# Optimization experiments

Hardware: AMD Instinct MI355X
Metric: run time of the kernel (lower is better)

Reference implementation:

```python
import jax, jax.numpy as jnp
import numpy as np
import math

B, S, H, K = 512, 200, 256, 16

def setup_inputs() -> dict:
    key = jax.random.key(0)
    ks = jax.random.split(key, 8)
    scale = 1.0 / math.sqrt(H)
    return {
        "input_tensor": jax.random.normal(ks[0], (B, S, H), dtype=jnp.float32),
        "item_mask": jax.random.randint(ks[1], (B, S, 1), 0, 2) > 0,
        "time_f_w_matrix": jax.random.uniform(ks[2], (B, S, 1), dtype=jnp.float32),
        "W1": jax.random.normal(ks[3], (H, H), dtype=jnp.float32) * scale,
        "b1": jnp.zeros((H,), dtype=jnp.float32),
        "W2": jax.random.normal(ks[4], (H, H), dtype=jnp.float32) * scale,
        "b2": jnp.zeros((H,), dtype=jnp.float32),
        "W3": jax.random.normal(ks[5], (H, K), dtype=jnp.float32) * scale,
    }

def reference(input_tensor, item_mask, time_f_w_matrix, W1, b1, W2, b2, W3):
    # small MLP: two Linear+ReLU then bias-free Linear to k_interests
    h = jax.nn.relu(jnp.einsum('bsh,hd->bsd', input_tensor, W1) + b1)
    h = jax.nn.relu(jnp.einsum('bsh,hd->bsd', h, W2) + b2)
    D = jnp.einsum('bsh,hk->bsk', h, W3)              # [B,S,K]
    D = jax.nn.softmax(D, axis=-1)                    # softmax over interests
    mask = item_mask[:, :, 0:1]                       # [B,S,1] bool, broadcast over K
    D = jnp.where(mask, D, jnp.float32(-10000.0))
    D = D / jnp.float32(math.sqrt(K))
    D = jax.nn.softmax(D, axis=-2)                    # softmax over sequence
    D = time_f_w_matrix[:, :, 0:1] * D                # time weighting
    # einsum 'nij,nik->nkj': pool items into K interest vectors
    return jnp.einsum('bsh,bsk->bkh', input_tensor, D)
```

## Files before the change

### kernel.cpp

```cpp
#include <hip/hip_runtime.h>
#include <math.h>

#define HDIM 256
#define KDIM 16
#define SDIM 200
#define BDIM 512
#define NROWS (BDIM * SDIM)
#define TM 64

typedef __bf16 bf16x8 __attribute__((ext_vector_type(8)));
typedef __bf16 bf16x4 __attribute__((ext_vector_type(4)));
typedef float  f32x4  __attribute__((ext_vector_type(4)));

__global__ __launch_bounds__(256) void pack_w_kernel(
    const float* __restrict__ src, __bf16* __restrict__ hi,
    __bf16* __restrict__ lo, int lgN)
{
    int idx = blockIdx.x * 256 + threadIdx.x;
    int N = 1 << lgN;
    int k = idx >> lgN;
    int n = idx & (N - 1);
    float v = src[idx];
    __bf16 h = (__bf16)v;
    float r = v - (float)h;
    int d = (((k >> 3) << lgN) + n) * 8 + (k & 7);
    hi[d] = h;
    lo[d] = (__bf16)r;
}

__global__ __launch_bounds__(256, 2) void mlp_softk_mfma(
    const float* __restrict__ X, const int* __restrict__ mask,
    const __bf16* __restrict__ W1h, const __bf16* __restrict__ W1l,
    const float* __restrict__ b1,
    const __bf16* __restrict__ W2h, const __bf16* __restrict__ W2l,
    const float* __restrict__ b2,
    const __bf16* __restrict__ W3h, const __bf16* __restrict__ W3l,
    float* __restrict__ P)
{
    __shared__ __bf16 Ahi[TM * HDIM];
    __shared__ __bf16 Alo[TM * HDIM];

    const int tid  = threadIdx.x;
    const int lane = tid & 63;
    const int w    = tid >> 6;
    const int l15  = lane & 15;
    const int quad = lane >> 4;
    const long r0  = (long)blockIdx.x * TM;

    {
        const float4* Xt = (const float4*)(X + r0 * HDIM);
        #pragma unroll
        for (int t = 0; t < (TM * HDIM / 4) / 256; ++t) {
            int v4  = tid + t * 256;
            float4 f = Xt[v4];
            int row = v4 >> 6;
            int col = (v4 & 63) << 2;
            int kgs = (col >> 3) ^ (row & 31);
            int base = row * HDIM + kgs * 8 + (col & 7);
            __bf16 h0 = (__bf16)f.x, h1 = (__bf16)f.y,
                   h2 = (__bf16)f.z, h3 = (__bf16)f.w;
            bf16x4 hv = {h0, h1, h2, h3};
            bf16x4 lv = {(__bf16)(f.x - (float)h0), (__bf16)(f.y - (float)h1),
                         (__bf16)(f.z - (float)h2), (__bf16)(f.w - (float)h3)};
            *(bf16x4*)(&Ahi[base]) = hv;
            *(bf16x4*)(&Alo[base]) = lv;
        }
    }
    __syncthreads();

    f32x4 acc[4][4];

    auto layer = [&](const __bf16* __restrict__ Wh, const __bf16* __restrict__ Wl,
                     const float* __restrict__ bias) {
        #pragma unroll
        for (int mt = 0; mt < 4; ++mt)
            #pragma unroll
            for (int nt = 0; nt < 4; ++nt)
                acc[mt][nt] = (f32x4){0.f, 0.f, 0.f, 0.f};

        #pragma unroll 2
        for (int kc = 0; kc < 8; ++kc) {
            bf16x8 ah[4], al[4], bh[4], bl[4];
            #pragma unroll
            for (int mt = 0; mt < 4; ++mt) {
                int row = mt * 16 + l15;
                int kgs = (kc * 4 + quad) ^ (row & 31);
                ah[mt] = *(const bf16x8*)(&Ahi[row * HDIM + kgs * 8]);
                al[mt] = *(const bf16x8*)(&Alo[row * HDIM + kgs * 8]);
            }
            #pragma unroll
            for (int nt = 0; nt < 4; ++nt) {
                int n  = w * 64 + nt * 16 + l15;
                int kg = kc * 4 + quad;
                bh[nt] = *(const bf16x8*)(Wh + (kg * HDIM + n) * 8);
                bl[nt] = *(const bf16x8*)(Wl + (kg * HDIM + n) * 8);
            }
            #pragma unroll
            for (int mt = 0; mt < 4; ++mt)
                #pragma unroll
                for (int nt = 0; nt < 4; ++nt) {
                    acc[mt][nt] = __builtin_amdgcn_mfma_f32_16x16x32_bf16(
                        ah[mt], bh[nt], acc[mt][nt], 0, 0, 0);
                    acc[mt][nt] = __builtin_amdgcn_mfma_f32_16x16x32_bf16(
                        al[mt], bh[nt], acc[mt][nt], 0, 0, 0);
                    acc[mt][nt] = __builtin_amdgcn_mfma_f32_16x16x32_bf16(
                        ah[mt], bl[nt], acc[mt][nt], 0, 0, 0);
                }
        }
        __syncthreads();

        float bias_v[4];
        #pragma unroll
        for (int nt = 0; nt < 4; ++nt) bias_v[nt] = bias[w * 64 + nt * 16 + l15];
        #pragma unroll
        for (int mt = 0; mt < 4; ++mt)
            #pragma unroll
            for (int nt = 0; nt < 4; ++nt)
                #pragma unroll
                for (int r = 0; r < 4; ++r) {
                    float v = fmaxf(acc[mt][nt][r] + bias_v[nt], 0.f);
                    int row = mt * 16 + quad * 4 + r;
                    int col = w * 64 + nt * 16 + l15;
                    int idx = row * HDIM + (((col >> 3) ^ (row & 31)) * 8) + (col & 7);
                    __bf16 h = (__bf16)v;
                    Ahi[idx] = h;
                    Alo[idx] = (__bf16)(v - (float)h);
                }
        __syncthreads();
    };

    layer(W1h, W1l, b1);
    layer(W2h, W2l, b2);

    f32x4 lg = {0.f, 0.f, 0.f, 0.f};
    #pragma unroll
    for (int kc = 0; kc < 8; ++kc) {
        int row = w * 16 + l15;
        int kg  = kc * 4 + quad;
        int kgs = kg ^ (row & 31);
        bf16x8 ah = *(const bf16x8*)(&Ahi[row * HDIM + kgs * 8]);
        bf16x8 al = *(const bf16x8*)(&Alo[row * HDIM + kgs * 8]);
        bf16x8 bh = *(const bf16x8*)(W3h + (kg * KDIM + l15) * 8);
        bf16x8 bl = *(const bf16x8*)(W3l + (kg * KDIM + l15) * 8);
        lg = __builtin_amdgcn_mfma_f32_16x16x32_bf16(ah, bh, lg, 0, 0, 0);
        lg = __builtin_amdgcn_mfma_f32_16x16x32_bf16(al, bh, lg, 0, 0, 0);
        lg = __builtin_amdgcn_mfma_f32_16x16x32_bf16(ah, bl, lg, 0, 0, 0);
    }

    #pragma unroll
    for (int r = 0; r < 4; ++r) {
        float v  = lg[r];
        float mx = v;
        mx = fmaxf(mx, __shfl_xor(mx, 1));
        mx = fmaxf(mx, __shfl_xor(mx, 2));
        mx = fmaxf(mx, __shfl_xor(mx, 4));
        mx = fmaxf(mx, __shfl_xor(mx, 8));
        float e = __expf(v - mx);
        float s = e;
        s += __shfl_xor(s, 1);
        s += __shfl_xor(s, 2);
        s += __shfl_xor(s, 4);
        s += __shfl_xor(s, 8);
        int grow = (int)r0 + w * 16 + quad * 4 + r;
        int mv   = mask[grow];
        float ov = mv ? (e / s) * 0.25f : -2500.0f;
        P[(long)grow * KDIM + l15] = ov;
    }
}

__global__ __launch_bounds__(256, 2) void softs_agg_kernel(
    const float* __restrict__ X, const float* __restrict__ tf,
    const float* __restrict__ P, float* __restrict__ out)
{
    __shared__ float wl[SDIM * KDIM];
    __shared__ float tfl[SDIM];
    __shared__ float psum[256];
    __shared__ float invk[KDIM];

    const int tid = threadIdx.x;
    const int b   = blockIdx.x;

    const float* Pb = P + (long)b * SDIM * KDIM;
    float ps = 0.f;
    #pragma unroll
    for (int t = 0; t < 13; ++t) {
        int i = tid + t * 256;
        if (i < SDIM * KDIM) {
            float e = __expf(Pb[i]);
            wl[i] = e;
            ps += e;
        }
    }
    psum[tid] = ps;
    if (tid < SDIM) tfl[tid] = tf[b * SDIM + tid];
    __syncthreads();

    if (tid < KDIM) {
        float s = 0.f;
        #pragma unroll
        for (int g = 0; g < 16; ++g) s += psum[tid + g * 16];
        invk[tid] = 1.f / s;
    }
    __syncthreads();

    #pragma unroll
    for (int t = 0; t < 13; ++t) {
        int i = tid + t * 256;
        if (i < SDIM * KDIM) wl[i] *= tfl[i >> 4] * invk[i & 15];
    }
    __syncthreads();

    const int w  = tid >> 6;
    const int ln = tid & 63;
    f32x4 acc[4];
    #pragma unroll
    for (int j = 0; j < 4; ++j) acc[j] = (f32x4){0.f, 0.f, 0.f, 0.f};

    const float4* Xb = (const float4*)(X + (long)b * SDIM * HDIM);
    for (int s = 0; s < SDIM; ++s) {
        float4 xv = Xb[s * 64 + ln];
        f32x4 x = {xv.x, xv.y, xv.z, xv.w};
        #pragma unroll
        for (int j = 0; j < 4; ++j) {
            float wt = wl[s * KDIM + 4 * w + j];
            acc[j] += x * wt;
        }
    }

    float4* Ob = (float4*)(out + (long)b * KDIM * HDIM);
    #pragma unroll
    for (int j = 0; j < 4; ++j) {
        float4 o = {acc[j][0], acc[j][1], acc[j][2], acc[j][3]};
        Ob[(4 * w + j) * 64 + ln] = o;
    }
}

extern "C" void kernel_launch(void* const* d_in, const int* in_sizes, int n_in,
                              void* d_out, int out_size, void* d_ws, size_t ws_size,
                              hipStream_t stream) {
    (void)in_sizes; (void)n_in; (void)out_size; (void)ws_size;
    const float* X    = (const float*)d_in[0];
    const int*   mask = (const int*)  d_in[1];
    const float* tf   = (const float*)d_in[2];
    const float* W1   = (const float*)d_in[3];
    const float* b1   = (const float*)d_in[4];
    const float* W2   = (const float*)d_in[5];
    const float* b2   = (const float*)d_in[6];
    const float* W3   = (const float*)d_in[7];
    float* out = (float*)d_out;

    char* ws = (char*)d_ws;
    float*  P   = (float*)ws;
    __bf16* w1h = (__bf16*)(ws + 6553600);
    __bf16* w1l = w1h + 65536;
    __bf16* w2h = w1l + 65536;
    __bf16* w2l = w2h + 65536;
    __bf16* w3h = w2l + 65536;
    __bf16* w3l = w3h + 4096;

    pack_w_kernel<<<256, 256, 0, stream>>>(W1, w1h, w1l, 8);
    pack_w_kernel<<<256, 256, 0, stream>>>(W2, w2h, w2l, 8);
    pack_w_kernel<<<16,  256, 0, stream>>>(W3, w3h, w3l, 4);
    mlp_softk_mfma<<<NROWS / TM, 256, 0, stream>>>(X, mask, w1h, w1l, b1,
                                                   w2h, w2l, b2, w3h, w3l, P);
    softs_agg_kernel<<<BDIM, 256, 0, stream>>>(X, tf, P, out);
}
```

Before: 276.1 us.

## Double-buffer MLP operand loads and restructure aggregation to per-column threads

The MLP layer loop now prefetches the next k-chunk's A (LDS) and B (global weight) fragments into a second register buffer while the MFMAs for the current chunk run. The goal is to hide load latency behind the matrix ops. Separately, the aggregation kernel now assigns each thread one hidden column with all 16 interest accumulators, reading X as scalars and the weights as LDS vector loads. This replaces four columns by four interests per thread, which cuts redundant LDS weight reads. The change raises register pressure in both kernels and drops the occupancy hint on the aggregation kernel.

```diff
diff --git a/kernel.cpp b/kernel.cpp
--- a/kernel.cpp
+++ b/kernel.cpp
@@ -78,33 +78,47 @@
             for (int nt = 0; nt < 4; ++nt)
                 acc[mt][nt] = (f32x4){0.f, 0.f, 0.f, 0.f};
 
-        #pragma unroll 2
-        for (int kc = 0; kc < 8; ++kc) {
-            bf16x8 ah[4], al[4], bh[4], bl[4];
+        bf16x8 ahb[2][4], alb[2][4], bhb[2][4], blb[2][4];
+
+        auto loadB = [&](int kc, int s) {
+            #pragma unroll
+            for (int nt = 0; nt < 4; ++nt) {
+                int n  = w * 64 + nt * 16 + l15;
+                int kg = kc * 4 + quad;
+                bhb[s][nt] = *(const bf16x8*)(Wh + (kg * HDIM + n) * 8);
+                blb[s][nt] = *(const bf16x8*)(Wl + (kg * HDIM + n) * 8);
+            }
+        };
+        auto loadA = [&](int kc, int s) {
             #pragma unroll
             for (int mt = 0; mt < 4; ++mt) {
                 int row = mt * 16 + l15;
                 int kgs = (kc * 4 + quad) ^ (row & 31);
-                ah[mt] = *(const bf16x8*)(&Ahi[row * HDIM + kgs * 8]);
-                al[mt] = *(const bf16x8*)(&Alo[row * HDIM + kgs * 8]);
+                ahb[s][mt] = *(const bf16x8*)(&Ahi[row * HDIM + kgs * 8]);
+                alb[s][mt] = *(const bf16x8*)(&Alo[row * HDIM + kgs * 8]);
             }
-            #pragma unroll
-            for (int nt = 0; nt < 4; ++nt) {
-                int n  = w * 64 + nt * 16 + l15;
-                int kg = kc * 4 + quad;
-                bh[nt] = *(const bf16x8*)(Wh + (kg * HDIM + n) * 8);
-                bl[nt] = *(const bf16x8*)(Wl + (kg * HDIM + n) * 8);
+        };
+
+        loadB(0, 0);
+        loadA(0, 0);
+
+        #pragma unroll
+        for (int kc = 0; kc < 8; ++kc) {
+            const int cur = kc & 1, nxt = cur ^ 1;
+            if (kc < 7) {
+                loadB(kc + 1, nxt);
+                loadA(kc + 1, nxt);
             }
             #pragma unroll
             for (int mt = 0; mt < 4; ++mt)
                 #pragma unroll
                 for (int nt = 0; nt < 4; ++nt) {
                     acc[mt][nt] = __builtin_amdgcn_mfma_f32_16x16x32_bf16(
-                        ah[mt], bh[nt], acc[mt][nt], 0, 0, 0);
+                        ahb[cur][mt], bhb[cur][nt], acc[mt][nt], 0, 0, 0);
                     acc[mt][nt] = __builtin_amdgcn_mfma_f32_16x16x32_bf16(
-                        al[mt], bh[nt], acc[mt][nt], 0, 0, 0);
+                        alb[cur][mt], bhb[cur][nt], acc[mt][nt], 0, 0, 0);
                     acc[mt][nt] = __builtin_amdgcn_mfma_f32_16x16x32_bf16(
-                        ah[mt], bl[nt], acc[mt][nt], 0, 0, 0);
+                        ahb[cur][mt], blb[cur][nt], acc[mt][nt], 0, 0, 0);
                 }
         }
         __syncthreads();
@@ -168,7 +182,7 @@
     }
 }
 
-__global__ __launch_bounds__(256, 2) void softs_agg_kernel(
+__global__ __launch_bounds__(256) void softs_agg_kernel(
     const float* __restrict__ X, const float* __restrict__ tf,
     const float* __restrict__ P, float* __restrict__ out)
 {
@@ -212,27 +226,32 @@
 
     const int w  = tid >> 6;
     const int ln = tid & 63;
-    f32x4 acc[4];
-    #pragma unroll
-    for (int j = 0; j < 4; ++j) acc[j] = (f32x4){0.f, 0.f, 0.f, 0.f};
-
-    const float4* Xb = (const float4*)(X + (long)b * SDIM * HDIM);
+    float acc[KDIM];
+    #pragma unroll
+    for (int k = 0; k < KDIM; ++k) acc[k] = 0.f;
+
+    const float* Xb  = X + (long)b * SDIM * HDIM + w * 64 + ln;
+    const f32x4* wl4 = (const f32x4*)wl;
+    #pragma unroll 4
     for (int s = 0; s < SDIM; ++s) {
-        float4 xv = Xb[s * 64 + ln];
-        f32x4 x = {xv.x, xv.y, xv.z, xv.w};
+        float x = Xb[(long)s * HDIM];
+        f32x4 d0 = wl4[s * 4 + 0];
+        f32x4 d1 = wl4[s * 4 + 1];
+        f32x4 d2 = wl4[s * 4 + 2];
+        f32x4 d3 = wl4[s * 4 + 3];
         #pragma unroll
         for (int j = 0; j < 4; ++j) {
-            float wt = wl[s * KDIM + 4 * w + j];
-            acc[j] += x * wt;
-        }
-    }
-
-    float4* Ob = (float4*)(out + (long)b * KDIM * HDIM);
-    #pragma unroll
-    for (int j = 0; j < 4; ++j) {
-        float4 o = {acc[j][0], acc[j][1], acc[j][2], acc[j][3]};
-        Ob[(4 * w + j) * 64 + ln] = o;
-    }
+            acc[0 + j]  = fmaf(x, d0[j], acc[0 + j]);
+            acc[4 + j]  = fmaf(x, d1[j], acc[4 + j]);
+            acc[8 + j]  = fmaf(x, d2[j], acc[8 + j]);
+            acc[12 + j] = fmaf(x, d3[j], acc[12 + j]);
+        }
+    }
+
+    float* ob = out + (long)b * KDIM * HDIM + w * 64 + ln;
+    #pragma unroll
+    for (int k = 0; k < KDIM; ++k)
+        ob[(long)k * HDIM] = acc[k];
 }
 
 extern "C" void kernel_launch(void* const* d_in, const int* in_sizes, int n_in,
```

New measurement: 341.2 us. 23.6% more time.

## Halve MLP row tile for occupancy and restructure aggregation over sequence halves

Applied to the files above, without the earlier changes.

The MLP kernel tile shrinks from 64 to 32 rows, with launch bounds raised to 4 blocks per CU. This halves LDS use and accumulator registers, but weights are fetched from global memory twice as often per row, and the final projection now runs on only two waves. The aggregation kernel is reorganised so each thread owns two hidden columns across all 16 interests. The 200-step sequence is split between wave pairs and the halves are combined through an LDS reduction. This removes the old pattern where all four waves reloaded the same X rows, and it reads the weights as broadcast vectors.

```diff
diff --git a/kernel.cpp b/kernel.cpp
--- a/kernel.cpp
+++ b/kernel.cpp
@@ -6,7 +6,7 @@
 #define SDIM 200
 #define BDIM 512
 #define NROWS (BDIM * SDIM)
-#define TM 64
+#define TM 32
 
 typedef __bf16 bf16x8 __attribute__((ext_vector_type(8)));
 typedef __bf16 bf16x4 __attribute__((ext_vector_type(4)));
@@ -28,7 +28,7 @@
     lo[d] = (__bf16)r;
 }
 
-__global__ __launch_bounds__(256, 2) void mlp_softk_mfma(
+__global__ __launch_bounds__(256, 4) void mlp_softk_mfma(
     const float* __restrict__ X, const int* __restrict__ mask,
     const __bf16* __restrict__ W1h, const __bf16* __restrict__ W1l,
     const float* __restrict__ b1,
@@ -68,26 +68,19 @@
     }
     __syncthreads();
 
-    f32x4 acc[4][4];
+    f32x4 acc[2][4];
 
     auto layer = [&](const __bf16* __restrict__ Wh, const __bf16* __restrict__ Wl,
                      const float* __restrict__ bias) {
         #pragma unroll
-        for (int mt = 0; mt < 4; ++mt)
+        for (int mt = 0; mt < 2; ++mt)
             #pragma unroll
             for (int nt = 0; nt < 4; ++nt)
                 acc[mt][nt] = (f32x4){0.f, 0.f, 0.f, 0.f};
 
         #pragma unroll 2
         for (int kc = 0; kc < 8; ++kc) {
-            bf16x8 ah[4], al[4], bh[4], bl[4];
-            #pragma unroll
-            for (int mt = 0; mt < 4; ++mt) {
-                int row = mt * 16 + l15;
-                int kgs = (kc * 4 + quad) ^ (row & 31);
-                ah[mt] = *(const bf16x8*)(&Ahi[row * HDIM + kgs * 8]);
-                al[mt] = *(const bf16x8*)(&Alo[row * HDIM + kgs * 8]);
-            }
+            bf16x8 bh[4], bl[4], ah[2], al[2];
             #pragma unroll
             for (int nt = 0; nt < 4; ++nt) {
                 int n  = w * 64 + nt * 16 + l15;
@@ -96,7 +89,14 @@
                 bl[nt] = *(const bf16x8*)(Wl + (kg * HDIM + n) * 8);
             }
             #pragma unroll
-            for (int mt = 0; mt < 4; ++mt)
+            for (int mt = 0; mt < 2; ++mt) {
+                int row = mt * 16 + l15;
+                int kgs = (kc * 4 + quad) ^ (row & 31);
+                ah[mt] = *(const bf16x8*)(&Ahi[row * HDIM + kgs * 8]);
+                al[mt] = *(const bf16x8*)(&Alo[row * HDIM + kgs * 8]);
+            }
+            #pragma unroll
+            for (int mt = 0; mt < 2; ++mt)
                 #pragma unroll
                 for (int nt = 0; nt < 4; ++nt) {
                     acc[mt][nt] = __builtin_amdgcn_mfma_f32_16x16x32_bf16(
@@ -113,7 +113,7 @@
         #pragma unroll
         for (int nt = 0; nt < 4; ++nt) bias_v[nt] = bias[w * 64 + nt * 16 + l15];
         #pragma unroll
-        for (int mt = 0; mt < 4; ++mt)
+        for (int mt = 0; mt < 2; ++mt)
             #pragma unroll
             for (int nt = 0; nt < 4; ++nt)
                 #pragma unroll
@@ -132,43 +132,45 @@
     layer(W1h, W1l, b1);
     layer(W2h, W2l, b2);
 
-    f32x4 lg = {0.f, 0.f, 0.f, 0.f};
-    #pragma unroll
-    for (int kc = 0; kc < 8; ++kc) {
-        int row = w * 16 + l15;
-        int kg  = kc * 4 + quad;
-        int kgs = kg ^ (row & 31);
-        bf16x8 ah = *(const bf16x8*)(&Ahi[row * HDIM + kgs * 8]);
-        bf16x8 al = *(const bf16x8*)(&Alo[row * HDIM + kgs * 8]);
-        bf16x8 bh = *(const bf16x8*)(W3h + (kg * KDIM + l15) * 8);
-        bf16x8 bl = *(const bf16x8*)(W3l + (kg * KDIM + l15) * 8);
-        lg = __builtin_amdgcn_mfma_f32_16x16x32_bf16(ah, bh, lg, 0, 0, 0);
-        lg = __builtin_amdgcn_mfma_f32_16x16x32_bf16(al, bh, lg, 0, 0, 0);
-        lg = __builtin_amdgcn_mfma_f32_16x16x32_bf16(ah, bl, lg, 0, 0, 0);
-    }
-
-    #pragma unroll
-    for (int r = 0; r < 4; ++r) {
-        float v  = lg[r];
-        float mx = v;
-        mx = fmaxf(mx, __shfl_xor(mx, 1));
-        mx = fmaxf(mx, __shfl_xor(mx, 2));
-        mx = fmaxf(mx, __shfl_xor(mx, 4));
-        mx = fmaxf(mx, __shfl_xor(mx, 8));
-        float e = __expf(v - mx);
-        float s = e;
-        s += __shfl_xor(s, 1);
-        s += __shfl_xor(s, 2);
-        s += __shfl_xor(s, 4);
-        s += __shfl_xor(s, 8);
-        int grow = (int)r0 + w * 16 + quad * 4 + r;
-        int mv   = mask[grow];
-        float ov = mv ? (e / s) * 0.25f : -2500.0f;
-        P[(long)grow * KDIM + l15] = ov;
-    }
-}
-
-__global__ __launch_bounds__(256, 2) void softs_agg_kernel(
+    if (w < 2) {
+        f32x4 lg = {0.f, 0.f, 0.f, 0.f};
+        #pragma unroll
+        for (int kc = 0; kc < 8; ++kc) {
+            int row = w * 16 + l15;
+            int kg  = kc * 4 + quad;
+            int kgs = kg ^ (row & 31);
+            bf16x8 ah = *(const bf16x8*)(&Ahi[row * HDIM + kgs * 8]);
+            bf16x8 al = *(const bf16x8*)(&Alo[row * HDIM + kgs * 8]);
+            bf16x8 bh = *(const bf16x8*)(W3h + (kg * KDIM + l15) * 8);
+            bf16x8 bl = *(const bf16x8*)(W3l + (kg * KDIM + l15) * 8);
+            lg = __builtin_amdgcn_mfma_f32_16x16x32_bf16(ah, bh, lg, 0, 0, 0);
+            lg = __builtin_amdgcn_mfma_f32_16x16x32_bf16(al, bh, lg, 0, 0, 0);
+            lg = __builtin_amdgcn_mfma_f32_16x16x32_bf16(ah, bl, lg, 0, 0, 0);
+        }
+
+        #pragma unroll
+        for (int r = 0; r < 4; ++r) {
+            float v  = lg[r];
+            float mx = v;
+            mx = fmaxf(mx, __shfl_xor(mx, 1));
+            mx = fmaxf(mx, __shfl_xor(mx, 2));
+            mx = fmaxf(mx, __shfl_xor(mx, 4));
+            mx = fmaxf(mx, __shfl_xor(mx, 8));
+            float e = __expf(v - mx);
+            float s = e;
+            s += __shfl_xor(s, 1);
+            s += __shfl_xor(s, 2);
+            s += __shfl_xor(s, 4);
+            s += __shfl_xor(s, 8);
+            int grow = (int)r0 + w * 16 + quad * 4 + r;
+            int mv   = mask[grow];
+            float ov = mv ? (e / s) * 0.25f : -2500.0f;
+            P[(long)grow * KDIM + l15] = ov;
+        }
+    }
+}
+
+__global__ __launch_bounds__(256) void softs_agg_kernel(
     const float* __restrict__ X, const float* __restrict__ tf,
     const float* __restrict__ P, float* __restrict__ out)
 {
@@ -176,6 +178,7 @@
     __shared__ float tfl[SDIM];
     __shared__ float psum[256];
     __shared__ float invk[KDIM];
+    __shared__ float red[KDIM * HDIM];
 
     const int tid = threadIdx.x;
     const int b   = blockIdx.x;
@@ -210,28 +213,56 @@
     }
     __syncthreads();
 
-    const int w  = tid >> 6;
+    const int wv = tid >> 6;
+    const int sh = wv >> 1;
+    const int hh = wv & 1;
     const int ln = tid & 63;
-    f32x4 acc[4];
+
+    float accx[KDIM], accy[KDIM];
     #pragma unroll
-    for (int j = 0; j < 4; ++j) acc[j] = (f32x4){0.f, 0.f, 0.f, 0.f};
-
-    const float4* Xb = (const float4*)(X + (long)b * SDIM * HDIM);
-    for (int s = 0; s < SDIM; ++s) {
-        float4 xv = Xb[s * 64 + ln];
-        f32x4 x = {xv.x, xv.y, xv.z, xv.w};
+    for (int k = 0; k < KDIM; ++k) { accx[k] = 0.f; accy[k] = 0.f; }
+
+    const float2* Xb  = (const float2*)(X + (long)b * SDIM * HDIM) + hh * 64 + ln;
+    const f32x4*  wl4 = (const f32x4*)wl;
+    const int s0 = sh * 100;
+    #pragma unroll 4
+    for (int si = 0; si < 100; ++si) {
+        int s = s0 + si;
+        float2 x = Xb[(long)s * (HDIM / 2)];
+        f32x4 d0 = wl4[s * 4 + 0];
+        f32x4 d1 = wl4[s * 4 + 1];
+        f32x4 d2 = wl4[s * 4 + 2];
+        f32x4 d3 = wl4[s * 4 + 3];
         #pragma unroll
         for (int j = 0; j < 4; ++j) {
-            float wt = wl[s * KDIM + 4 * w + j];
-            acc[j] += x * wt;
-        }
-    }
-
-    float4* Ob = (float4*)(out + (long)b * KDIM * HDIM);
-    #pragma unroll
-    for (int j = 0; j < 4; ++j) {
-        float4 o = {acc[j][0], acc[j][1], acc[j][2], acc[j][3]};
-        Ob[(4 * w + j) * 64 + ln] = o;
+            accx[0 + j]  = fmaf(x.x, d0[j], accx[0 + j]);
+            accx[4 + j]  = fmaf(x.x, d1[j], accx[4 + j]);
+            accx[8 + j]  = fmaf(x.x, d2[j], accx[8 + j]);
+            accx[12 + j] = fmaf(x.x, d3[j], accx[12 + j]);
+            accy[0 + j]  = fmaf(x.y, d0[j], accy[0 + j]);
+            accy[4 + j]  = fmaf(x.y, d1[j], accy[4 + j]);
+            accy[8 + j]  = fmaf(x.y, d2[j], accy[8 + j]);
+            accy[12 + j] = fmaf(x.y, d3[j], accy[12 + j]);
+        }
+    }
+
+    if (sh == 1) {
+        #pragma unroll
+        for (int k = 0; k < KDIM; ++k) {
+            red[k * HDIM + hh * 128 + 2 * ln + 0] = accx[k];
+            red[k * HDIM + hh * 128 + 2 * ln + 1] = accy[k];
+        }
+    }
+    __syncthreads();
+    if (sh == 0) {
+        float* ob = out + (long)b * KDIM * HDIM + hh * 128 + 2 * ln;
+        #pragma unroll
+        for (int k = 0; k < KDIM; ++k) {
+            float2 o;
+            o.x = accx[k] + red[k * HDIM + hh * 128 + 2 * ln + 0];
+            o.y = accy[k] + red[k * HDIM + hh * 128 + 2 * ln + 1];
+            *(float2*)(ob + (long)k * HDIM) = o;
+        }
     }
 }
 
```

Measured after the change: 285.2 us. 1.03x slower.
